# Optimization experiments

Measured on AMD Instinct MI355X. Metric: run time of the kernel, lower is better.

The kernel has to match this reference:

```python
import jax, jax.numpy as jnp
import numpy as np

NEG_INF = -1e38

def wkv(w, u, k, v):
    """Numerically-stable RWKV-4 WKV recurrence.
    w, u: [C] (log-space decay / first-token bonus)
    k, v: [B, T, C]
    returns y: [B, T, C]
    """
    B, T, C = k.shape

    def step(carry, kv):
        p, q, o = carry          # numerator state, denominator state, running log-max; each [B, C]
        kt, vt = kv              # [B, C]
        # output at t (includes the u-boosted current token)
        no = jnp.maximum(o, u + kt)
        A = jnp.exp(o - no)
        Bt = jnp.exp(u + kt - no)
        y = (A * p + Bt * vt) / (A * q + Bt)
        # state update (decay by w, absorb current token)
        no2 = jnp.maximum(w + o, kt)
        A2 = jnp.exp(w + o - no2)
        B2 = jnp.exp(kt - no2)
        return (A2 * p + B2 * vt, A2 * q + B2, no2), y

    init = (jnp.zeros((B, C), k.dtype), jnp.zeros((B, C), k.dtype),
            jnp.full((B, C), NEG_INF, k.dtype))
    kT = jnp.swapaxes(k, 0, 1)   # [T, B, C]
    vT = jnp.swapaxes(v, 0, 1)
    _, ys = jax.lax.scan(step, init, (kT, vT))
    return jnp.swapaxes(ys, 0, 1)


def setup_inputs() -> dict:
    key = jax.random.key(0)
    ks = jax.random.split(key, 10)
    B, T, C = 8, 4096, 512
    scale = 1.0 / np.sqrt(C)
    return {
        "x": jax.random.normal(ks[0], (B, T, C), jnp.float32),
        "spatial_decay": jax.random.normal(ks[1], (C,), jnp.float32),
        "spatial_first": jax.random.normal(ks[2], (C,), jnp.float32),
        "mix_k": jax.random.uniform(ks[3], (1, 1, C), jnp.float32),
        "mix_v": jax.random.uniform(ks[4], (1, 1, C), jnp.float32),
        "mix_r": jax.random.uniform(ks[5], (1, 1, C), jnp.float32),
        "wk": jax.random.normal(ks[6], (C, C), jnp.float32) * scale,
        "wv": jax.random.normal(ks[7], (C, C), jnp.float32) * scale,
        "wr": jax.random.normal(ks[8], (C, C), jnp.float32) * scale,
        "wo": jax.random.normal(ks[9], (C, C), jnp.float32) * scale,
    }


def reference(x, spatial_decay, spatial_first, mix_k, mix_v, mix_r, wk, wv, wr, wo):
    B, T, C = x.shape
    # time_shift: xx[t] = x[t-1], xx[0] = 0  (ZeroPad2d((0,0,1,-1)))
    xx = jnp.pad(x, ((0, 0), (1, 0), (0, 0)))[:, :-1]
    xk = x * mix_k + xx * (1.0 - mix_k)
    xv = x * mix_v + xx * (1.0 - mix_v)
    xr = x * mix_r + xx * (1.0 - mix_r)
    k = jnp.einsum('btc,cd->btd', xk, wk)
    v = jnp.einsum('btc,cd->btd', xv, wv)
    r = jnp.einsum('btc,cd->btd', xr, wr)
    sr = jax.nn.sigmoid(r)
    y = wkv(spatial_decay / T, spatial_first / T, k, v)
    return jnp.einsum('btc,cd->btd', sr * y, wo)
```

## Files before the change

### kernel.cpp

```cpp
#include <hip/hip_runtime.h>

#define BB 8
#define TT 4096
#define CC 512
#define MM (BB * TT)
#define SS 128
#define LL 32

typedef short short8 __attribute__((ext_vector_type(8)));
typedef unsigned short ushort8 __attribute__((ext_vector_type(8)));
typedef float f32x4 __attribute__((ext_vector_type(4)));

__device__ __forceinline__ unsigned short f2bf(float f) {
    unsigned int u = __float_as_uint(f);
    u += 0x7FFFu + ((u >> 16) & 1u);
    return (unsigned short)(u >> 16);
}
__device__ __forceinline__ float bf2f(unsigned short h) {
    return __uint_as_float(((unsigned int)h) << 16);
}

__device__ __forceinline__ void gl_lds16(const void* g, void* l) {
    __builtin_amdgcn_global_load_lds(
        (__attribute__((address_space(1))) void*)(unsigned long long)g,
        (__attribute__((address_space(3))) void*)(unsigned int)(unsigned long long)l,
        16, 0, 0);
}

__device__ __forceinline__ ushort8 pack8(f32x4 a, f32x4 b) {
    ushort8 r;
    r[0] = f2bf(a.x); r[1] = f2bf(a.y); r[2] = f2bf(a.z); r[3] = f2bf(a.w);
    r[4] = f2bf(b.x); r[5] = f2bf(b.y); r[6] = f2bf(b.z); r[7] = f2bf(b.w);
    return r;
}

__global__ void transpose_w(const float* __restrict__ wk, const float* __restrict__ wv,
                            const float* __restrict__ wr, const float* __restrict__ wo,
                            unsigned short* __restrict__ wT) {
    const int which = blockIdx.y;
    const float* src = (which == 0) ? wk : (which == 1) ? wv : (which == 2) ? wr : wo;
    const int i = blockIdx.x * 256 + threadIdx.x;
    const int n = i >> 9;
    const int k = i & 511;
    wT[(size_t)which * (CC * CC) + i] = f2bf(src[(size_t)k * CC + n]);
}

__global__ __launch_bounds__(256) void mix_kvr(
    const float* __restrict__ x,
    const float* __restrict__ mixk, const float* __restrict__ mixv,
    const float* __restrict__ mixr,
    unsigned short* __restrict__ kx, unsigned short* __restrict__ vx,
    unsigned short* __restrict__ rx) {
    const int idx = blockIdx.x * 256 + threadIdx.x;
    const int row = idx >> 6;
    const int ch  = (idx & 63) * 8;
    const int t   = row & (TT - 1);
    const size_t off = (size_t)row * CC + ch;
    const float* xr = x + off;

    const f32x4 zero4 = {0.f, 0.f, 0.f, 0.f};
    const f32x4 one4  = {1.f, 1.f, 1.f, 1.f};

    f32x4 xc0 = ((const f32x4*)xr)[0];
    f32x4 xc1 = ((const f32x4*)xr)[1];
    f32x4 xp0 = zero4, xp1 = zero4;
    if (t != 0) {
        xp0 = ((const f32x4*)(xr - CC))[0];
        xp1 = ((const f32x4*)(xr - CC))[1];
    }

    f32x4 m0, m1;
    m0 = ((const f32x4*)(mixk + ch))[0];
    m1 = ((const f32x4*)(mixk + ch))[1];
    *(ushort8*)(kx + off) = pack8(xc0 * m0 + xp0 * (one4 - m0),
                                  xc1 * m1 + xp1 * (one4 - m1));
    m0 = ((const f32x4*)(mixv + ch))[0];
    m1 = ((const f32x4*)(mixv + ch))[1];
    *(ushort8*)(vx + off) = pack8(xc0 * m0 + xp0 * (one4 - m0),
                                  xc1 * m1 + xp1 * (one4 - m1));
    m0 = ((const f32x4*)(mixr + ch))[0];
    m1 = ((const f32x4*)(mixr + ch))[1];
    *(ushort8*)(rx + off) = pack8(xc0 * m0 + xp0 * (one4 - m0),
                                  xc1 * m1 + xp1 * (one4 - m1));
}

#define STAGE_KVR(bufidx, k0) do {                                              \
    gl_lds16(agA + (k0), &As[bufidx][tid * 8]);                                 \
    gl_lds16(agA + (size_t)64 * CC + (k0), &As[bufidx][(256 + tid) * 8]);       \
    _Pragma("unroll")                                                           \
    for (int s_ = 0; s_ < 4; ++s_)                                              \
        gl_lds16(agB + (size_t)(s_ * 64) * CC + (k0),                           \
                 &Bs[bufidx][(s_ * 256 + tid) * 8]);                            \
} while (0)

__global__ __launch_bounds__(256, 2) void gemm_tile(
    const unsigned short* __restrict__ A,
    const unsigned short* __restrict__ Bw,
    unsigned short* __restrict__ Out,
    const int sig) {
    __shared__ unsigned short As[2][128 * 32];
    __shared__ unsigned short Bs[2][256 * 32];

    const int tid = threadIdx.x;
    const int pm = blockIdx.x;
    const int pn = blockIdx.y;

    const int ar = tid >> 2;
    const int cg = (tid & 3) ^ ((tid >> 3) & 3);
    const unsigned short* agA = A  + (size_t)(pm * 128 + ar) * CC + cg * 8;
    const unsigned short* agB = Bw + (size_t)(pn * 256 + ar) * CC + cg * 8;

    const int w = tid >> 6, lane = tid & 63;
    const int wr = w >> 1, wc = w & 1;
    const int q = lane >> 4, l16 = lane & 15;
    const int sw = (q ^ ((l16 >> 1) & 3)) * 8;

    f32x4 acc[4][8];
#pragma unroll
    for (int i = 0; i < 4; i++)
#pragma unroll
        for (int j = 0; j < 8; j++) acc[i][j] = (f32x4){0.f, 0.f, 0.f, 0.f};

    STAGE_KVR(0, 0);
    __syncthreads();

    for (int kt = 0; kt < 16; ++kt) {
        const int cur = kt & 1;
        if (kt + 1 < 16) {
            const int nxt = cur ^ 1;
            const int k0 = (kt + 1) * 32;
            STAGE_KVR(nxt, k0);
        }

        short8 a[4], b[8];
#pragma unroll
        for (int i = 0; i < 4; i++)
            a[i] = *(const short8*)&As[cur][(wr * 64 + i * 16 + l16) * 32 + sw];
#pragma unroll
        for (int j = 0; j < 8; j++)
            b[j] = *(const short8*)&Bs[cur][(wc * 128 + j * 16 + l16) * 32 + sw];
#pragma unroll
        for (int i = 0; i < 4; i++)
#pragma unroll
            for (int j = 0; j < 8; j++)
                acc[i][j] = __builtin_amdgcn_mfma_f32_16x16x32_bf16(a[i], b[j], acc[i][j], 0, 0, 0);

        __syncthreads();
    }

    const size_t rb = (size_t)pm * 128 + wr * 64;
    const int nb = pn * 256 + wc * 128;
#pragma unroll
    for (int i = 0; i < 4; i++)
#pragma unroll
        for (int j = 0; j < 8; j++)
#pragma unroll
            for (int ii = 0; ii < 4; ii++) {
                const int m = i * 16 + q * 4 + ii;
                const int n = nb + j * 16 + l16;
                float val = acc[i][j][ii];
                if (sig) val = 1.0f / (1.0f + __expf(-val));
                Out[(rb + m) * CC + n] = f2bf(val);
            }
}

__global__ __launch_bounds__(256) void wkv_part1(
    const unsigned short* __restrict__ kb, const unsigned short* __restrict__ vb,
    const float* __restrict__ sd,
    float* __restrict__ sp_, float* __restrict__ sq_, float* __restrict__ so_) {
    const int idx = blockIdx.x * 256 + threadIdx.x;
    const int c = idx & (CC - 1);
    const int b = (idx >> 9) & (BB - 1);
    const int s = idx >> 12;
    const float w = sd[c] * (1.0f / (float)TT);
    const size_t base = ((size_t)b * TT + (size_t)s * LL) * CC + c;
    const unsigned short* kp = kb + base;
    const unsigned short* vp = vb + base;

    float p = 0.f, q = 0.f, o = -1e38f;
#pragma unroll 8
    for (int i = 0; i < LL; ++i) {
        const float kt = bf2f(kp[(size_t)i * CC]);
        const float vt = bf2f(vp[(size_t)i * CC]);
        const float no2 = fmaxf(w + o, kt);
        const float A2  = __expf(w + o - no2);
        const float B2  = __expf(kt - no2);
        p = A2 * p + B2 * vt;
        q = A2 * q + B2;
        o = no2;
    }
    sp_[idx] = p; sq_[idx] = q; so_[idx] = o;
}

__global__ __launch_bounds__(256) void wkv_part2(
    const float* __restrict__ sd,
    float* __restrict__ sp_, float* __restrict__ sq_, float* __restrict__ so_) {
    const int idx = blockIdx.x * 256 + threadIdx.x;
    const int c = idx & (CC - 1);
    const float wL = sd[c] * ((float)LL / (float)TT);

    float p = 0.f, q = 0.f, o = -1e38f;
    float lp = sp_[idx], lq = sq_[idx], lo = so_[idx];
    for (int s = 0; s < SS; ++s) {
        const int off = s * (BB * CC) + idx;
        float nlp = 0.f, nlq = 0.f, nlo = 0.f;
        if (s + 1 < SS) {
            nlp = sp_[off + BB * CC];
            nlq = sq_[off + BB * CC];
            nlo = so_[off + BB * CC];
        }
        sp_[off] = p; sq_[off] = q; so_[off] = o;
        const float no = fmaxf(o + wL, lo);
        const float A  = __expf(o + wL - no);
        const float Bc = __expf(lo - no);
        p = A * p + Bc * lp;
        q = A * q + Bc * lq;
        o = no;
        lp = nlp; lq = nlq; lo = nlo;
    }
}

__global__ __launch_bounds__(256) void wkv_part3(
    const unsigned short* __restrict__ kb, const unsigned short* __restrict__ vb,
    const unsigned short* __restrict__ srb,
    const float* __restrict__ sd, const float* __restrict__ sf,
    const float* __restrict__ sp_, const float* __restrict__ sq_,
    const float* __restrict__ so_,
    unsigned short* __restrict__ zb) {
    const int idx = blockIdx.x * 256 + threadIdx.x;
    const int c = idx & (CC - 1);
    const int b = (idx >> 9) & (BB - 1);
    const int s = idx >> 12;
    const float w = sd[c] * (1.0f / (float)TT);
    const float u = sf[c] * (1.0f / (float)TT);
    const size_t base = ((size_t)b * TT + (size_t)s * LL) * CC + c;
    const unsigned short* kp = kb + base;
    const unsigned short* vp = vb + base;
    const unsigned short* sp = srb + base;
    unsigned short* zp = zb + base;

    float p = sp_[idx], q = sq_[idx], o = so_[idx];
#pragma unroll 4
    for (int i = 0; i < LL; ++i) {
        const float kt = bf2f(kp[(size_t)i * CC]);
        const float vt = bf2f(vp[(size_t)i * CC]);
        const float sr = bf2f(sp[(size_t)i * CC]);

        const float no = fmaxf(o, u + kt);
        const float A  = __expf(o - no);
        const float Bt = __expf(u + kt - no);
        const float y  = (A * p + Bt * vt) / (A * q + Bt);
        zp[(size_t)i * CC] = f2bf(sr * y);

        const float no2 = fmaxf(w + o, kt);
        const float A2  = __expf(w + o - no2);
        const float B2  = __expf(kt - no2);
        p = A2 * p + B2 * vt;
        q = A2 * q + B2;
        o = no2;
    }
}

__global__ __launch_bounds__(256, 2) void gemm_out(
    const unsigned short* __restrict__ zb, const unsigned short* __restrict__ woT,
    float* __restrict__ out) {
    __shared__ unsigned short As[2][128 * 32];
    __shared__ unsigned short Bs[2][256 * 32];

    const int tid = threadIdx.x;
    const int pm = blockIdx.x;
    const int pn = blockIdx.y;

    const int ar = tid >> 2;
    const int cg = (tid & 3) ^ ((tid >> 3) & 3);
    const unsigned short* agA = zb  + (size_t)(pm * 128 + ar) * CC + cg * 8;
    const unsigned short* agB = woT + (size_t)(pn * 256 + ar) * CC + cg * 8;

    const int w = tid >> 6, lane = tid & 63;
    const int wr = w >> 1, wc = w & 1;
    const int q = lane >> 4, l16 = lane & 15;
    const int sw = (q ^ ((l16 >> 1) & 3)) * 8;

    f32x4 acc[4][8];
#pragma unroll
    for (int i = 0; i < 4; i++)
#pragma unroll
        for (int j = 0; j < 8; j++) acc[i][j] = (f32x4){0.f, 0.f, 0.f, 0.f};

    STAGE_KVR(0, 0);
    __syncthreads();

    for (int kt = 0; kt < 16; ++kt) {
        const int cur = kt & 1;
        if (kt + 1 < 16) {
            const int nxt = cur ^ 1;
            const int k0 = (kt + 1) * 32;
            STAGE_KVR(nxt, k0);
        }

        short8 a[4], b[8];
#pragma unroll
        for (int i = 0; i < 4; i++)
            a[i] = *(const short8*)&As[cur][(wr * 64 + i * 16 + l16) * 32 + sw];
#pragma unroll
        for (int j = 0; j < 8; j++)
            b[j] = *(const short8*)&Bs[cur][(wc * 128 + j * 16 + l16) * 32 + sw];
#pragma unroll
        for (int i = 0; i < 4; i++)
#pragma unroll
            for (int j = 0; j < 8; j++)
                acc[i][j] = __builtin_amdgcn_mfma_f32_16x16x32_bf16(a[i], b[j], acc[i][j], 0, 0, 0);

        __syncthreads();
    }

    const size_t rb = (size_t)pm * 128 + wr * 64;
    const int nb = pn * 256 + wc * 128;
#pragma unroll
    for (int i = 0; i < 4; i++)
#pragma unroll
        for (int j = 0; j < 8; j++)
#pragma unroll
            for (int ii = 0; ii < 4; ii++) {
                const int m = i * 16 + q * 4 + ii;
                const int n = nb + j * 16 + l16;
                out[(rb + m) * CC + n] = acc[i][j][ii];
            }
}

extern "C" void kernel_launch(void* const* d_in, const int* in_sizes, int n_in,
                              void* d_out, int out_size, void* d_ws, size_t ws_size,
                              hipStream_t stream) {
    const float* x  = (const float*)d_in[0];
    const float* sd = (const float*)d_in[1];
    const float* sf = (const float*)d_in[2];
    const float* mk = (const float*)d_in[3];
    const float* mv = (const float*)d_in[4];
    const float* mr = (const float*)d_in[5];
    const float* wk = (const float*)d_in[6];
    const float* wv = (const float*)d_in[7];
    const float* wr = (const float*)d_in[8];
    const float* wo = (const float*)d_in[9];
    float* out = (float*)d_out;

    char* ws = (char*)d_ws;
    unsigned short* wT = (unsigned short*)ws;
    unsigned short* b1 = (unsigned short*)(ws + (size_t)4 * CC * CC * 2);
    unsigned short* b2 = b1 + (size_t)MM * CC;
    unsigned short* b3 = b2 + (size_t)MM * CC;
    unsigned short* b4 = b3 + (size_t)MM * CC;
    float* sp_ = (float*)(b4 + (size_t)MM * CC);
    float* sq_ = sp_ + (size_t)SS * BB * CC;
    float* so_ = sq_ + (size_t)SS * BB * CC;
    unsigned short* woT = wT + (size_t)3 * CC * CC;

    transpose_w<<<dim3((CC * CC) / 256, 4), 256, 0, stream>>>(wk, wv, wr, wo, wT);

    mix_kvr<<<dim3((MM * CC / 8) / 256), 256, 0, stream>>>(
        x, mk, mv, mr, b1, b2, b3);

    gemm_tile<<<dim3(MM / 128, 2), 256, 0, stream>>>(b1, wT + (size_t)0 * CC * CC, b4, 0);
    gemm_tile<<<dim3(MM / 128, 2), 256, 0, stream>>>(b2, wT + (size_t)1 * CC * CC, b1, 0);
    gemm_tile<<<dim3(MM / 128, 2), 256, 0, stream>>>(b3, wT + (size_t)2 * CC * CC, b2, 1);

    wkv_part1<<<dim3((SS * BB * CC) / 256), 256, 0, stream>>>(b4, b1, sd, sp_, sq_, so_);
    wkv_part2<<<dim3((BB * CC) / 256), 256, 0, stream>>>(sd, sp_, sq_, so_);
    wkv_part3<<<dim3((SS * BB * CC) / 256), 256, 0, stream>>>(
        b4, b1, b2, sd, sf, sp_, sq_, so_, b3);

    gemm_out<<<dim3(MM / 128, 2), 256, 0, stream>>>(b3, woT, out);
}
```

Before: 318.6 us.

## Triple-buffer GEMM pipeline, merge kvr GEMMs into one launch, tile weight transpose

The GEMM mainloop moves from double to triple buffering with explicit vmcnt waits and raw barriers, and raises wave priority around the MFMA block. The three k/v/r projection GEMMs become a single launch over a z grid dimension, with the block index remapped so that consecutive blocks spread across groups. The weight transpose now goes through a padded LDS tile so both reads and writes are coalesced. The sigmoid(r) buffer is parked in the output buffer as scratch. The cost is 50% more LDS per block, which may cut occupancy, and hand-counted waitcnt values that depend on exactly six loads per stage.

```diff
diff --git a/kernel.cpp b/kernel.cpp
--- a/kernel.cpp
+++ b/kernel.cpp
@@ -34,15 +34,25 @@
     return r;
 }
 
-__global__ void transpose_w(const float* __restrict__ wk, const float* __restrict__ wv,
-                            const float* __restrict__ wr, const float* __restrict__ wo,
-                            unsigned short* __restrict__ wT) {
-    const int which = blockIdx.y;
+__global__ __launch_bounds__(256) void transpose_w(
+    const float* __restrict__ wk, const float* __restrict__ wv,
+    const float* __restrict__ wr, const float* __restrict__ wo,
+    unsigned short* __restrict__ wT) {
+    __shared__ float t[64][65];
+    const int which = blockIdx.z;
     const float* src = (which == 0) ? wk : (which == 1) ? wv : (which == 2) ? wr : wo;
-    const int i = blockIdx.x * 256 + threadIdx.x;
-    const int n = i >> 9;
-    const int k = i & 511;
-    wT[(size_t)which * (CC * CC) + i] = f2bf(src[(size_t)k * CC + n]);
+    const int k0 = blockIdx.y * 64;
+    const int n0 = blockIdx.x * 64;
+    const int r = threadIdx.x >> 6;
+    const int c = threadIdx.x & 63;
+#pragma unroll
+    for (int p = 0; p < 16; ++p)
+        t[p * 4 + r][c] = src[(size_t)(k0 + p * 4 + r) * CC + n0 + c];
+    __syncthreads();
+    unsigned short* dst = wT + (size_t)which * (CC * CC);
+#pragma unroll
+    for (int p = 0; p < 16; ++p)
+        dst[(size_t)(n0 + p * 4 + r) * CC + k0 + c] = f2bf(t[c][p * 4 + r]);
 }
 
 __global__ __launch_bounds__(256) void mix_kvr(
@@ -84,27 +94,16 @@
                                   xc1 * m1 + xp1 * (one4 - m1));
 }
 
-#define STAGE_KVR(bufidx, k0) do {                                              \
-    gl_lds16(agA + (k0), &As[bufidx][tid * 8]);                                 \
-    gl_lds16(agA + (size_t)64 * CC + (k0), &As[bufidx][(256 + tid) * 8]);       \
-    _Pragma("unroll")                                                           \
-    for (int s_ = 0; s_ < 4; ++s_)                                              \
-        gl_lds16(agB + (size_t)(s_ * 64) * CC + (k0),                           \
-                 &Bs[bufidx][(s_ * 256 + tid) * 8]);                            \
-} while (0)
-
-__global__ __launch_bounds__(256, 2) void gemm_tile(
+template <bool F32OUT>
+__device__ __forceinline__ void gemm_body(
     const unsigned short* __restrict__ A,
     const unsigned short* __restrict__ Bw,
-    unsigned short* __restrict__ Out,
-    const int sig) {
-    __shared__ unsigned short As[2][128 * 32];
-    __shared__ unsigned short Bs[2][256 * 32];
+    void* __restrict__ OutP, const int sig,
+    const int pm, const int pn) {
+    __shared__ unsigned short As[3][128 * 32];
+    __shared__ unsigned short Bs[3][256 * 32];
 
     const int tid = threadIdx.x;
-    const int pm = blockIdx.x;
-    const int pn = blockIdx.y;
-
     const int ar = tid >> 2;
     const int cg = (tid & 3) ^ ((tid >> 3) & 3);
     const unsigned short* agA = A  + (size_t)(pm * 128 + ar) * CC + cg * 8;
@@ -121,47 +120,100 @@
 #pragma unroll
         for (int j = 0; j < 8; j++) acc[i][j] = (f32x4){0.f, 0.f, 0.f, 0.f};
 
-    STAGE_KVR(0, 0);
-    __syncthreads();
-
+#define STG(bi, k0) do {                                                        \
+    gl_lds16(agA + (k0), &As[bi][tid * 8]);                                     \
+    gl_lds16(agA + (size_t)64 * CC + (k0), &As[bi][(256 + tid) * 8]);           \
+    gl_lds16(agB + (k0),                    &Bs[bi][(0 * 256 + tid) * 8]);      \
+    gl_lds16(agB + (size_t)64  * CC + (k0), &Bs[bi][(1 * 256 + tid) * 8]);      \
+    gl_lds16(agB + (size_t)128 * CC + (k0), &Bs[bi][(2 * 256 + tid) * 8]);      \
+    gl_lds16(agB + (size_t)192 * CC + (k0), &Bs[bi][(3 * 256 + tid) * 8]);      \
+} while (0)
+
+    STG(0, 0);
+    STG(1, 32);
+
+#pragma unroll
     for (int kt = 0; kt < 16; ++kt) {
-        const int cur = kt & 1;
-        if (kt + 1 < 16) {
-            const int nxt = cur ^ 1;
-            const int k0 = (kt + 1) * 32;
-            STAGE_KVR(nxt, k0);
-        }
+        const int bi = kt % 3;
+        if (kt + 2 < 16) STG((kt + 2) % 3, (kt + 2) * 32);
+
+        if (kt < 14)       asm volatile("s_waitcnt vmcnt(12)" ::: "memory");
+        else if (kt == 14) asm volatile("s_waitcnt vmcnt(6)" ::: "memory");
+        else               asm volatile("s_waitcnt vmcnt(0)" ::: "memory");
+        __builtin_amdgcn_s_barrier();
 
         short8 a[4], b[8];
 #pragma unroll
         for (int i = 0; i < 4; i++)
-            a[i] = *(const short8*)&As[cur][(wr * 64 + i * 16 + l16) * 32 + sw];
+            a[i] = *(const short8*)&As[bi][(wr * 64 + i * 16 + l16) * 32 + sw];
 #pragma unroll
         for (int j = 0; j < 8; j++)
-            b[j] = *(const short8*)&Bs[cur][(wc * 128 + j * 16 + l16) * 32 + sw];
+            b[j] = *(const short8*)&Bs[bi][(wc * 128 + j * 16 + l16) * 32 + sw];
+        asm volatile("s_waitcnt lgkmcnt(0)" ::: "memory");
+        __builtin_amdgcn_s_barrier();
+
+        __builtin_amdgcn_s_setprio(1);
 #pragma unroll
         for (int i = 0; i < 4; i++)
 #pragma unroll
             for (int j = 0; j < 8; j++)
                 acc[i][j] = __builtin_amdgcn_mfma_f32_16x16x32_bf16(a[i], b[j], acc[i][j], 0, 0, 0);
-
-        __syncthreads();
-    }
+        __builtin_amdgcn_s_setprio(0);
+    }
+#undef STG
 
     const size_t rb = (size_t)pm * 128 + wr * 64;
     const int nb = pn * 256 + wc * 128;
-#pragma unroll
-    for (int i = 0; i < 4; i++)
-#pragma unroll
-        for (int j = 0; j < 8; j++)
-#pragma unroll
-            for (int ii = 0; ii < 4; ii++) {
-                const int m = i * 16 + q * 4 + ii;
-                const int n = nb + j * 16 + l16;
-                float val = acc[i][j][ii];
-                if (sig) val = 1.0f / (1.0f + __expf(-val));
-                Out[(rb + m) * CC + n] = f2bf(val);
-            }
+    if constexpr (F32OUT) {
+        float* Out = (float*)OutP;
+#pragma unroll
+        for (int i = 0; i < 4; i++)
+#pragma unroll
+            for (int j = 0; j < 8; j++)
+#pragma unroll
+                for (int ii = 0; ii < 4; ii++) {
+                    const int m = i * 16 + q * 4 + ii;
+                    const int n = nb + j * 16 + l16;
+                    Out[(rb + m) * CC + n] = acc[i][j][ii];
+                }
+    } else {
+        unsigned short* Out = (unsigned short*)OutP;
+#pragma unroll
+        for (int i = 0; i < 4; i++)
+#pragma unroll
+            for (int j = 0; j < 8; j++)
+#pragma unroll
+                for (int ii = 0; ii < 4; ii++) {
+                    const int m = i * 16 + q * 4 + ii;
+                    const int n = nb + j * 16 + l16;
+                    float val = acc[i][j][ii];
+                    if (sig) val = 1.0f / (1.0f + __expf(-val));
+                    Out[(rb + m) * CC + n] = f2bf(val);
+                }
+    }
+}
+
+__global__ __launch_bounds__(256, 2) void gemm_kvr3(
+    const unsigned short* __restrict__ wT,
+    const unsigned short* __restrict__ A0, const unsigned short* __restrict__ A1,
+    const unsigned short* __restrict__ A2,
+    unsigned short* __restrict__ O0, unsigned short* __restrict__ O1,
+    unsigned short* __restrict__ O2) {
+    const int z = blockIdx.y;
+    const int lin = blockIdx.x;
+    const int wg = (lin & 7) * 64 + (lin >> 3);
+    const int pm = wg >> 1, pn = wg & 1;
+    const unsigned short* A = (z == 0) ? A0 : (z == 1) ? A1 : A2;
+    unsigned short* O = (z == 0) ? O0 : (z == 1) ? O1 : O2;
+    gemm_body<false>(A, wT + (size_t)z * (CC * CC), O, z == 2, pm, pn);
+}
+
+__global__ __launch_bounds__(256, 2) void gemm_out(
+    const unsigned short* __restrict__ zb, const unsigned short* __restrict__ woT,
+    float* __restrict__ out) {
+    const int lin = blockIdx.x;
+    const int wg = (lin & 7) * 64 + (lin >> 3);
+    gemm_body<true>(zb, woT, out, 0, wg >> 1, wg & 1);
 }
 
 __global__ __launch_bounds__(256) void wkv_part1(
@@ -261,73 +313,6 @@
     }
 }
 
-__global__ __launch_bounds__(256, 2) void gemm_out(
-    const unsigned short* __restrict__ zb, const unsigned short* __restrict__ woT,
-    float* __restrict__ out) {
-    __shared__ unsigned short As[2][128 * 32];
-    __shared__ unsigned short Bs[2][256 * 32];
-
-    const int tid = threadIdx.x;
-    const int pm = blockIdx.x;
-    const int pn = blockIdx.y;
-
-    const int ar = tid >> 2;
-    const int cg = (tid & 3) ^ ((tid >> 3) & 3);
-    const unsigned short* agA = zb  + (size_t)(pm * 128 + ar) * CC + cg * 8;
-    const unsigned short* agB = woT + (size_t)(pn * 256 + ar) * CC + cg * 8;
-
-    const int w = tid >> 6, lane = tid & 63;
-    const int wr = w >> 1, wc = w & 1;
-    const int q = lane >> 4, l16 = lane & 15;
-    const int sw = (q ^ ((l16 >> 1) & 3)) * 8;
-
-    f32x4 acc[4][8];
-#pragma unroll
-    for (int i = 0; i < 4; i++)
-#pragma unroll
-        for (int j = 0; j < 8; j++) acc[i][j] = (f32x4){0.f, 0.f, 0.f, 0.f};
-
-    STAGE_KVR(0, 0);
-    __syncthreads();
-
-    for (int kt = 0; kt < 16; ++kt) {
-        const int cur = kt & 1;
-        if (kt + 1 < 16) {
-            const int nxt = cur ^ 1;
-            const int k0 = (kt + 1) * 32;
-            STAGE_KVR(nxt, k0);
-        }
-
-        short8 a[4], b[8];
-#pragma unroll
-        for (int i = 0; i < 4; i++)
-            a[i] = *(const short8*)&As[cur][(wr * 64 + i * 16 + l16) * 32 + sw];
-#pragma unroll
-        for (int j = 0; j < 8; j++)
-            b[j] = *(const short8*)&Bs[cur][(wc * 128 + j * 16 + l16) * 32 + sw];
-#pragma unroll
-        for (int i = 0; i < 4; i++)
-#pragma unroll
-            for (int j = 0; j < 8; j++)
-                acc[i][j] = __builtin_amdgcn_mfma_f32_16x16x32_bf16(a[i], b[j], acc[i][j], 0, 0, 0);
-
-        __syncthreads();
-    }
-
-    const size_t rb = (size_t)pm * 128 + wr * 64;
-    const int nb = pn * 256 + wc * 128;
-#pragma unroll
-    for (int i = 0; i < 4; i++)
-#pragma unroll
-        for (int j = 0; j < 8; j++)
-#pragma unroll
-            for (int ii = 0; ii < 4; ii++) {
-                const int m = i * 16 + q * 4 + ii;
-                const int n = nb + j * 16 + l16;
-                out[(rb + m) * CC + n] = acc[i][j][ii];
-            }
-}
-
 extern "C" void kernel_launch(void* const* d_in, const int* in_sizes, int n_in,
                               void* d_out, int out_size, void* d_ws, size_t ws_size,
                               hipStream_t stream) {
@@ -345,28 +330,28 @@
 
     char* ws = (char*)d_ws;
     unsigned short* wT = (unsigned short*)ws;
-    unsigned short* b1 = (unsigned short*)(ws + (size_t)4 * CC * CC * 2);
+    unsigned short* b1 = wT + (size_t)4 * CC * CC;
     unsigned short* b2 = b1 + (size_t)MM * CC;
     unsigned short* b3 = b2 + (size_t)MM * CC;
     unsigned short* b4 = b3 + (size_t)MM * CC;
-    float* sp_ = (float*)(b4 + (size_t)MM * CC);
+    unsigned short* b5 = b4 + (size_t)MM * CC;
+    float* sp_ = (float*)(b5 + (size_t)MM * CC);
     float* sq_ = sp_ + (size_t)SS * BB * CC;
     float* so_ = sq_ + (size_t)SS * BB * CC;
     unsigned short* woT = wT + (size_t)3 * CC * CC;
-
-    transpose_w<<<dim3((CC * CC) / 256, 4), 256, 0, stream>>>(wk, wv, wr, wo, wT);
+    unsigned short* srS = (unsigned short*)d_out;
+
+    transpose_w<<<dim3(8, 8, 4), 256, 0, stream>>>(wk, wv, wr, wo, wT);
 
     mix_kvr<<<dim3((MM * CC / 8) / 256), 256, 0, stream>>>(
         x, mk, mv, mr, b1, b2, b3);
 
-    gemm_tile<<<dim3(MM / 128, 2), 256, 0, stream>>>(b1, wT + (size_t)0 * CC * CC, b4, 0);
-    gemm_tile<<<dim3(MM / 128, 2), 256, 0, stream>>>(b2, wT + (size_t)1 * CC * CC, b1, 0);
-    gemm_tile<<<dim3(MM / 128, 2), 256, 0, stream>>>(b3, wT + (size_t)2 * CC * CC, b2, 1);
-
-    wkv_part1<<<dim3((SS * BB * CC) / 256), 256, 0, stream>>>(b4, b1, sd, sp_, sq_, so_);
+    gemm_kvr3<<<dim3(512, 3), 256, 0, stream>>>(wT, b1, b2, b3, b4, b5, srS);
+
+    wkv_part1<<<dim3((SS * BB * CC) / 256), 256, 0, stream>>>(b4, b5, sd, sp_, sq_, so_);
     wkv_part2<<<dim3((BB * CC) / 256), 256, 0, stream>>>(sd, sp_, sq_, so_);
     wkv_part3<<<dim3((SS * BB * CC) / 256), 256, 0, stream>>>(
-        b4, b1, b2, sd, sf, sp_, sq_, so_, b3);
-
-    gemm_out<<<dim3(MM / 128, 2), 256, 0, stream>>>(b3, woT, out);
-}
+        b4, b5, srS, sd, sf, sp_, sq_, so_, b1);
+
+    gemm_out<<<dim3(512), 256, 0, stream>>>(b1, woT, out);
+}
```

New measurement: 295.6 us. 1.08x faster.
